# Kernel tuning notes

Measured on AMD Instinct MI355X. Metric: run time of the kernel, lower is better.

## Reference

```python
import jax, jax.numpy as jnp
import numpy as np

N, E, B = 50000, 200000, 512
F0, H1, C2, EMB = 78, 10, 128, 128
SEQ, VOCAB, NF, KW = 1000, 26, 32, 8
LOUT = EMB - KW + 1  # 121


def setup_inputs() -> dict:
    key = jax.random.key(0)
    ks = jax.random.split(key, 20)
    nrm = lambda k, s: jax.random.normal(k, s, jnp.float32) * 0.05
    return dict(
        x=jax.random.normal(ks[0], (N, F0), jnp.float32),
        edge_index=jax.random.randint(ks[1], (2, E), 0, N),
        batch=(jnp.arange(N) * B) // N,  # balanced sorted node->graph ids, all segments non-empty
        target=jax.random.randint(ks[2], (B, SEQ), 0, VOCAB),
        W1=nrm(ks[3], (F0, H1 * F0)), a_src1=nrm(ks[4], (H1, F0)), a_dst1=nrm(ks[5], (H1, F0)), b1=jnp.zeros((H1 * F0,), jnp.float32),
        W2=nrm(ks[6], (H1 * F0, C2)), a_src2=nrm(ks[7], (1, C2)), a_dst2=nrm(ks[8], (1, C2)), b2=jnp.zeros((C2,), jnp.float32),
        fc_g1_w=nrm(ks[9], (C2, C2)), fc_g1_b=jnp.zeros((C2,), jnp.float32),
        emb=nrm(ks[10], (VOCAB, EMB)),
        conv_w=nrm(ks[11], (NF, SEQ, KW)), conv_b=jnp.zeros((NF,), jnp.float32),
        fc_xt_w=nrm(ks[12], (NF * LOUT, C2)), fc_xt_b=jnp.zeros((C2,), jnp.float32),
        fc1_w=nrm(ks[13], (2 * C2, 1024)), fc1_b=jnp.zeros((1024,), jnp.float32),
        fc2_w=nrm(ks[14], (1024, 256)), fc2_b=jnp.zeros((256,), jnp.float32),
        out_w=nrm(ks[15], (256, 1)), out_b=jnp.zeros((1,), jnp.float32),
    )


def gat_conv(x, src, dst, W, a_src, a_dst, b, heads):
    # PyG GATConv (eval mode): project, per-edge attn logits, segment softmax over dst, scatter-add
    n = x.shape[0]
    c = W.shape[1] // heads
    h = (x @ W).reshape(n, heads, c)                 # [N,H,C]
    al_s = (h * a_src).sum(-1)                       # [N,H]
    al_d = (h * a_dst).sum(-1)
    al = jax.nn.leaky_relu(al_s[src] + al_d[dst], 0.2)   # [E',H]
    amax = jax.ops.segment_max(al, dst, num_segments=n)
    ex = jnp.exp(al - amax[dst])
    den = jax.ops.segment_sum(ex, dst, num_segments=n)
    alpha = ex / (den[dst] + 1e-16)
    out = jax.ops.segment_sum(h[src] * alpha[:, :, None], dst, num_segments=n)  # [N,H,C]
    return out.reshape(n, heads * c) + b


def reference(x, edge_index, batch, target, W1, a_src1, a_dst1, b1, W2, a_src2, a_dst2, b2,
              fc_g1_w, fc_g1_b, emb, conv_w, conv_b, fc_xt_w, fc_xt_b,
              fc1_w, fc1_b, fc2_w, fc2_b, out_w, out_b):
    n = x.shape[0]
    loops = jnp.arange(n)
    src = jnp.concatenate([edge_index[0], loops])    # add self loops (PyG default)
    dst = jnp.concatenate([edge_index[1], loops])
    h = jax.nn.elu(gat_conv(x, src, dst, W1, a_src1, a_dst1, b1, H1))
    h = jax.nn.relu(gat_conv(h, src, dst, W2, a_src2, a_dst2, b2, 1))
    g = jax.ops.segment_max(h, batch, num_segments=B)            # global max pool per graph
    g = jax.nn.relu(g @ fc_g1_w + fc_g1_b)                       # [B,128]
    e = emb[target]                                              # [B,1000,128]
    conv = jax.lax.conv_general_dilated(e, conv_w, (1,), 'VALID',
                                        dimension_numbers=('NCH', 'OIH', 'NCH'))
    conv = jax.nn.relu(conv + conv_b[None, :, None])             # [B,32,121]
    xt = conv.reshape(B, NF * LOUT) @ fc_xt_w + fc_xt_b          # [B,128]
    xc = jnp.concatenate([g, xt], axis=1)                        # [B,256]
    xc = jax.nn.relu(xc @ fc1_w + fc1_b)
    xc = jax.nn.relu(xc @ fc2_w + fc2_b)
    return xc @ out_w + out_b                                    # [B,1]
```

## Files before the change

### kernel.cpp

```cpp
#include <hip/hip_runtime.h>
#include <hip/hip_bf16.h>

#define N_NODES 50000
#define N_EDGES 200000
#define BGRAPHS 512
#define F0c 78
#define H1c 10
#define HC1 780
#define HSTR 832
#define C2c 128
#define SEQc 1000
#define VOCABc 26
#define NFc 32
#define KWc 8
#define LOUTc 121
#define EMBc 128
#define KX 96
#define KXT 3872
#define KSTEPS2 13
#define MROWS 13312
#define KM 1024

typedef __attribute__((ext_vector_type(8))) short short8;
typedef __attribute__((ext_vector_type(4))) float f32x4;
typedef unsigned short u16;

static constexpr size_t alignup(size_t x) { return (x + 255) & ~size_t(255); }

static constexpr size_t A_HBUF = 0;
static constexpr size_t A_OUT1 = alignup(A_HBUF + size_t(N_NODES)*HSTR*2);
static constexpr size_t A_H2   = alignup(A_OUT1 + size_t(N_NODES)*HSTR*2);
static constexpr size_t A_W2T  = alignup(A_H2   + size_t(N_NODES)*C2c*4);
static constexpr size_t A_ALS1 = alignup(A_W2T  + size_t(C2c)*HSTR*2);
static constexpr size_t A_ALD1 = alignup(A_ALS1 + size_t(N_NODES)*H1c*4);
static constexpr size_t A_ALS2 = alignup(A_ALD1 + size_t(N_NODES)*H1c*4);
static constexpr size_t A_ALD2 = alignup(A_ALS2 + size_t(N_NODES)*4);
static constexpr size_t A_DEG  = alignup(A_ALD2 + size_t(N_NODES)*4);
static constexpr size_t A_OFFS = alignup(A_DEG  + size_t(N_NODES)*4);
static constexpr size_t A_CUR  = alignup(A_OFFS + size_t(N_NODES+1)*4);
static constexpr size_t A_CSRC = alignup(A_CUR  + size_t(N_NODES)*4);
static constexpr size_t A_XC   = alignup(A_CSRC + size_t(N_EDGES+N_NODES)*4);
static constexpr size_t A_Y1   = alignup(A_XC   + size_t(BGRAPHS)*256*4);
static constexpr size_t A_BOFF = alignup(A_Y1   + size_t(BGRAPHS)*1024*4);
static constexpr size_t A_BPAD = alignup(A_BOFF + size_t(BGRAPHS)*(VOCABc+1)*4);
static constexpr size_t A_WXT  = alignup(A_BPAD + size_t(HSTR)*4);
static constexpr size_t A_FXP  = alignup(A_WXT  + size_t(C2c)*KXT*2);
static constexpr size_t A_W1HP = alignup(A_FXP  + size_t(11)*BGRAPHS*C2c*4);
static constexpr size_t A_WSD  = alignup(A_W1HP + size_t(10)*80*96*2);
static constexpr size_t A_CWT  = alignup(A_WSD  + size_t(2)*H1c*F0c*4);
static constexpr size_t A_END  = alignup(A_CWT  + size_t(2)*256*KM*2);

static constexpr size_t A_HFIN = A_HBUF;
static constexpr size_t A_AMAT = alignup(A_HFIN + size_t(N_NODES)*C2c*4);
static constexpr size_t A_CVO  = alignup(A_AMAT + size_t(MROWS)*256*4);
static constexpr size_t A_M    = alignup(A_CVO  + size_t(BGRAPHS)*KXT*2);
static_assert(A_M + size_t(MROWS)*KM*2 <= size_t(N_NODES)*HSTR*2, "alias A overflow");
static constexpr size_t A_XPAD = A_OUT1;
static_assert(size_t(N_NODES)*KX*2 <= size_t(N_NODES)*HSTR*2, "alias B overflow");

__device__ __forceinline__ float bflo(unsigned u) { return __uint_as_float(u << 16); }
__device__ __forceinline__ float bfhi(unsigned u) { return __uint_as_float(u & 0xffff0000u); }
__device__ __forceinline__ u16 f2bf(float v) {
    __hip_bfloat16 b = __float2bfloat16(v);
    return *(u16*)&b;
}

#define GLOAD16(g, l) __builtin_amdgcn_global_load_lds( \
    (const __attribute__((address_space(1))) void*)(g), \
    (__attribute__((address_space(3))) void*)(l), 16, 0, 0)

__global__ void k_prep(const float* __restrict__ x, const float* __restrict__ W1,
                       const float* __restrict__ W2, const float* __restrict__ b1,
                       const float* __restrict__ fcxt_w, const float* __restrict__ conv_w,
                       const float* __restrict__ a_src1, const float* __restrict__ a_dst1,
                       __hip_bfloat16* __restrict__ xpad, __hip_bfloat16* __restrict__ w1hp,
                       __hip_bfloat16* __restrict__ w2t, float* __restrict__ bpad,
                       __hip_bfloat16* __restrict__ wxt, float* __restrict__ wsd,
                       u16* __restrict__ cwt, int* __restrict__ deg) {
    int i = blockIdx.x*256 + threadIdx.x;
    const int R0 = N_NODES;
    const int R1 = R0 + N_NODES*KX;
    const int R2 = R1 + 10*80*96;
    const int R3 = R2 + C2c*HSTR;
    const int R4 = R3 + HSTR;
    const int R5 = R4 + C2c*KXT;
    const int R6 = R5 + 2*H1c*F0c;
    const int R7 = R6 + 256*KM;
    if (i < R0) {
        deg[i] = 1;
    } else if (i < R1) {
        int t = i - R0; int n = t / KX, c = t - n*KX;
        xpad[t] = __float2bfloat16(c < F0c ? x[(size_t)n*F0c + c] : 0.f);
    } else if (i < R2) {
        int t = i - R1; int hh = t / 7680, rem = t - hh*7680;
        int j = rem / 96, k = rem - j*96;
        w1hp[t] = __float2bfloat16((j < F0c && k < F0c) ? W1[(size_t)k*HC1 + hh*F0c + j] : 0.f);
    } else if (i < R3) {
        int t = i - R2; int c = t / HSTR, p = t - c*HSTR;
        int hh = p / 80, cc = p - hh*80;
        w2t[t] = __float2bfloat16((hh < H1c && cc < F0c) ? W2[(size_t)(hh*F0c + cc)*C2c + c] : 0.f);
    } else if (i < R4) {
        int p = i - R3; int hh = p / 80, cc = p - hh*80;
        bpad[p] = (hh < H1c && cc < F0c) ? b1[hh*F0c + cc] : 0.f;
    } else if (i < R5) {
        int t = i - R4; int c = t / KXT, j = t - c*KXT;
        wxt[t] = __float2bfloat16(fcxt_w[(size_t)j*C2c + c]);
    } else if (i < R6) {
        int t = i - R5; int sd = t / (H1c*F0c), rem = t - sd*(H1c*F0c);
        int hh = rem / F0c, c = rem - hh*F0c;
        const float* a = sd ? a_dst1 : a_src1;
        float v = 0.f;
        for (int j = 0; j < F0c; j++) v += W1[(size_t)c*HC1 + hh*F0c + j] * a[hh*F0c + j];
        wsd[t] = v;
    } else if (i < R7) {
        int t = i - R6; int col = t >> 10, ii = t & (KM-1);
        int o = col >> 3, k = col & 7;
        float v = (ii < SEQc) ? conv_w[((size_t)o*SEQc + ii)*KWc + k] : 0.f;
        u16 h = f2bf(v);
        float hv = __uint_as_float((unsigned)h << 16);
        cwt[(size_t)col*KM + ii] = h;
        cwt[(size_t)256*KM + (size_t)col*KM + ii] = f2bf(v - hv);
    }
}
#define PREP_TOTAL (N_NODES + N_NODES*KX + 10*80*96 + C2c*HSTR + HSTR + C2c*KXT + 2*H1c*F0c + 256*KM)

__global__ void k_count(const int* __restrict__ ei, int* deg) {
    int i = blockIdx.x*256 + threadIdx.x;
    if (i < N_EDGES) atomicAdd(&deg[ei[N_EDGES + i]], 1);
}
__global__ void k_scan(const int* __restrict__ deg, int* __restrict__ off,
                       int* __restrict__ cur, int n) {
    __shared__ int wsum[16];
    __shared__ int s_carry;
    int tid = threadIdx.x, lane = tid & 63, wid = tid >> 6;
    if (tid == 0) s_carry = 0;
    __syncthreads();
    for (int base = 0; base < n; base += 1024) {
        int i = base + tid;
        int v0 = (i < n) ? deg[i] : 0;
        int v = v0;
        for (int d = 1; d < 64; d <<= 1) { int t = __shfl_up(v, d, 64); if (lane >= d) v += t; }
        if (lane == 63) wsum[wid] = v;
        __syncthreads();
        if (wid == 0) {
            int w = (lane < 16) ? wsum[lane] : 0;
            for (int d = 1; d < 16; d <<= 1) { int t = __shfl_up(w, d, 64); if (lane >= d) w += t; }
            if (lane < 16) wsum[lane] = w;
        }
        __syncthreads();
        int wprev = (wid > 0) ? wsum[wid-1] : 0;
        int carry = s_carry;
        if (i < n) { int o = carry + wprev + (v - v0); off[i] = o; cur[i] = o; }
        __syncthreads();
        if (tid == 0) s_carry = carry + wsum[15];
        __syncthreads();
    }
    if (tid == 0) off[n] = s_carry;
}
__global__ void k_fill(const int* __restrict__ ei, int* cur, int* __restrict__ csrc) {
    int i = blockIdx.x*256 + threadIdx.x;
    if (i < N_EDGES) {
        int s = ei[i], d = ei[N_EDGES + i];
        int p = atomicAdd(&cur[d], 1);
        csrc[p] = s;
    } else if (i < N_EDGES + N_NODES) {
        int n = i - N_EDGES;
        int p = atomicAdd(&cur[n], 1);
        csrc[p] = n;
    }
}
__global__ void k_sortcsr(const int* __restrict__ offs, int* __restrict__ csrc) {
    int n = blockIdx.x*256 + threadIdx.x;
    if (n >= N_NODES) return;
    int s = offs[n], e = offs[n+1];
    for (int i = s + 1; i < e; i++) {
        int v = csrc[i];
        int j = i - 1;
        while (j >= s && csrc[j] > v) { csrc[j+1] = csrc[j]; j--; }
        csrc[j+1] = v;
    }
}

__global__ void k_att1x(const float* __restrict__ x, const float* __restrict__ wsd,
                        float* __restrict__ als, float* __restrict__ ald) {
    int i = blockIdx.x*256 + threadIdx.x;
    if (i >= N_NODES*H1c) return;
    int n = i / H1c, hh = i - n*H1c;
    const float* xr = x + (size_t)n*F0c;
    const float* ws = wsd + hh*F0c;
    const float* wd = wsd + H1c*F0c + hh*F0c;
    float s1 = 0.f, s2 = 0.f;
    for (int c = 0; c < F0c; c++) { float v = xr[c]; s1 += v*ws[c]; s2 += v*wd[c]; }
    als[i] = s1; ald[i] = s2;
}

__global__ void k_agg1x(const unsigned* __restrict__ xpu, const float* __restrict__ als,
                        const float* __restrict__ ald, const int* __restrict__ offs,
                        const int* __restrict__ csrc, unsigned* __restrict__ xaggu) {
    constexpr int H = H1c;
    int dn = blockIdx.x, lane = threadIdx.x;
    int s = offs[dn], e = offs[dn+1], deg = e - s;
    __shared__ float wexp[64*H];
    __shared__ int   ssrc[64];
    __shared__ float ms[H], dinv_s[H];

    if (deg <= 64) {
        if (lane < deg) ssrc[lane] = csrc[s + lane];
        __syncthreads();
        for (int idx = lane; idx < deg*H; idx += 64) {
            int j = idx / H, hh = idx - j*H;
            float al = als[(size_t)ssrc[j]*H + hh] + ald[(size_t)dn*H + hh];
            wexp[idx] = (al >= 0.f) ? al : 0.2f*al;
        }
        __syncthreads();
        if (lane < H) {
            float m = -1e30f;
            for (int j = 0; j < deg; j++) m = fmaxf(m, wexp[j*H + lane]);
            float den = 0.f;
            for (int j = 0; j < deg; j++) den += __expf(wexp[j*H + lane] - m);
            ms[lane] = m; dinv_s[lane] = 1.f/(den + 1e-16f);
        }
        __syncthreads();
        for (int idx = lane; idx < deg*H; idx += 64) {
            int hh = idx % H;
            wexp[idx] = __expf(wexp[idx] - ms[hh]) * dinv_s[hh];
        }
        __syncthreads();
        if (lane < 40) {
            float accL[H], accH[H];
            #pragma unroll
            for (int hh = 0; hh < H; hh++) { accL[hh] = 0.f; accH[hh] = 0.f; }
            int j = 0;
            for (; j + 1 < deg; j += 2) {
                unsigned ua = xpu[(size_t)ssrc[j]*48 + lane];
                unsigned ub = xpu[(size_t)ssrc[j+1]*48 + lane];
                float a0 = bflo(ua), a1 = bfhi(ua), b0 = bflo(ub), b1 = bfhi(ub);
                #pragma unroll
                for (int hh = 0; hh < H; hh++) {
                    float wA = wexp[j*H + hh], wB = wexp[(j+1)*H + hh];
                    accL[hh] += wA*a0 + wB*b0;
                    accH[hh] += wA*a1 + wB*b1;
                }
            }
            if (j < deg) {
                unsigned ua = xpu[(size_t)ssrc[j]*48 + lane];
                float a0 = bflo(ua), a1 = bfhi(ua);
                #pragma unroll
                for (int hh = 0; hh < H; hh++) {
                    float wA = wexp[j*H + hh];
                    accL[hh] += wA*a0;
                    accH[hh] += wA*a1;
                }
            }
            #pragma unroll
            for (int hh = 0; hh < H; hh++) {
                unsigned p = (unsigned)f2bf(accL[hh]) | ((unsigned)f2bf(accH[hh]) << 16);
                xaggu[((size_t)dn*H + hh)*40 + lane] = p;
            }
        }
    } else {
        if (lane < H) {
            float adv = ald[(size_t)dn*H + lane];
            float m = -1e30f;
            for (int j = s; j < e; j++) {
                float al = als[(size_t)csrc[j]*H + lane] + adv;
                al = (al >= 0.f) ? al : 0.2f*al;
                m = fmaxf(m, al);
            }
            float den = 0.f;
            for (int j = s; j < e; j++) {
                float al = als[(size_t)csrc[j]*H + lane] + adv;
                al = (al >= 0.f) ? al : 0.2f*al;
                den += __expf(al - m);
            }
            ms[lane] = m; dinv_s[lane] = 1.f/(den + 1e-16f);
        }
        __syncthreads();
        if (lane < 40) {
            float accL[H], accH[H];
            #pragma unroll
            for (int hh = 0; hh < H; hh++) { accL[hh] = 0.f; accH[hh] = 0.f; }
            for (int j = s; j < e; j++) {
                int sj = csrc[j];
                unsigned ua = xpu[(size_t)sj*48 + lane];
                float a0 = bflo(ua), a1 = bfhi(ua);
                #pragma unroll
                for (int hh = 0; hh < H; hh++) {
                    float al = als[(size_t)sj*H + hh] + ald[(size_t)dn*H + hh];
                    al = (al >= 0.f) ? al : 0.2f*al;
                    float a = __expf(al - ms[hh]) * dinv_s[hh];
                    accL[hh] += a*a0;
                    accH[hh] += a*a1;
                }
            }
            #pragma unroll
            for (int hh = 0; hh < H; hh++) {
                unsigned p = (unsigned)f2bf(accL[hh]) | ((unsigned)f2bf(accH[hh]) << 16);
                xaggu[((size_t)dn*H + hh)*40 + lane] = p;
            }
        }
    }
}

__global__ void __launch_bounds__(512, 1)
k_fuse12(const short* __restrict__ xagg, const short* __restrict__ w1hp,
         const float* __restrict__ bpad, const short* __restrict__ Bt,
         const float* __restrict__ a_src2, const float* __restrict__ a_dst2,
         float* __restrict__ Cout, float* __restrict__ als2, float* __restrict__ ald2) {
    __shared__ __attribute__((aligned(16))) short As[64*832];
    __shared__ __attribute__((aligned(16))) short Bs[2][128*64];
    __shared__ float sred[64][4], sredd[64][4];
    int tid = threadIdx.x;
    int wave = tid >> 6, lane = tid & 63;
    int m16 = lane & 15, quad = lane >> 4;
    int blockrow = blockIdx.x * 64;

    size_t boff2[2];
    #pragma unroll
    for (int j = 0; j < 2; j++) {
        int c = wave*64 + j*512 + lane;
        int row = c >> 3, cb = (c & 7) << 4;
        boff2[j] = (size_t)row*(HSTR*2) + (cb ^ ((row & 7) << 4));
        GLOAD16((const char*)Bt + boff2[j], &Bs[0][(wave*64 + j*512)*8]);
    }

    {
        int wg = (wave >> 1) * 16;
        int h0 = (wave & 1) * 5;
        int rowc = min(blockrow + wg + m16, N_NODES-1);
        for (int hh = h0; hh < h0 + 5; hh++) {
            const short8* arow = (const short8*)(xagg + ((size_t)rowc*H1c + hh)*80);
            f32x4 acc1[5];
            #pragma unroll
            for (int ct = 0; ct < 5; ct++) acc1[ct] = (f32x4){0.f,0.f,0.f,0.f};
            #pragma unroll
            for (int kt = 0; kt < 3; kt++) {
                short8 af = arow[kt*4 + quad];
                #pragma unroll
                for (int ct = 0; ct < 5; ct++) {
                    const short8* brow = (const short8*)(w1hp + (size_t)(hh*80 + ct*16 + m16)*96);
                    acc1[ct] = __builtin_amdgcn_mfma_f32_16x16x32_bf16(af, brow[kt*4 + quad],
                                                                      acc1[ct], 0, 0, 0);
                }
            }
            #pragma unroll
            for (int ct = 0; ct < 5; ct++) {
                int col = hh*80 + ct*16 + m16;
                float bv = bpad[col];
                #pragma unroll
                for (int r = 0; r < 4; r++) {
                    int rl = wg + quad*4 + r;
                    float v = acc1[ct][r] + bv;
                    v = (v > 0.f) ? v : (__expf(v) - 1.f);
                    *(u16*)((char*)As + rl*1664 + ((col*2) ^ ((rl & 7) << 4))) = f2bf(v);
                }
            }
        }
    }
    for (int e = tid; e < 64*32; e += 512) {
        int rl = e >> 5, cc = 800 + (e & 31);
        *(u16*)((char*)As + rl*1664 + ((cc*2) ^ ((rl & 7) << 4))) = 0;
    }
    __syncthreads();

    int rg = (wave >> 2) * 32;
    int ch = (wave & 3) * 32;
    f32x4 acc[2][2];
    #pragma unroll
    for (int wr = 0; wr < 2; wr++)
        #pragma unroll
        for (int ct = 0; ct < 2; ct++) acc[wr][ct] = (f32x4){0.f,0.f,0.f,0.f};

    int S = (m16 & 7) << 4;
    int cur = 0;
    for (int s = 0; s < KSTEPS2; s++) {
        if (s + 1 < KSTEPS2) {
            size_t kb = (size_t)(s + 1) * 128;
            #pragma unroll
            for (int j = 0; j < 2; j++)
                GLOAD16((const char*)Bt + boff2[j] + kb, &Bs[cur^1][(wave*64 + j*512)*8]);
        }
        const char* asB = (const char*)As + (size_t)s*128;
        const char* bsB = (const char*)&Bs[cur][0];
        #pragma unroll
        for (int kk = 0; kk < 2; kk++) {
            int kb2 = (kk*64 + quad*16) ^ S;
            short8 af[2], bfv[2];
            #pragma unroll
            for (int wr = 0; wr < 2; wr++)
                af[wr] = *(const short8*)(asB + (rg + wr*16 + m16)*1664 + kb2);
            #pragma unroll
            for (int ct = 0; ct < 2; ct++)
                bfv[ct] = *(const short8*)(bsB + (ch + ct*16 + m16)*128 + kb2);
            #pragma unroll
            for (int wr = 0; wr < 2; wr++)
                #pragma unroll
                for (int ct = 0; ct < 2; ct++)
                    acc[wr][ct] = __builtin_amdgcn_mfma_f32_16x16x32_bf16(af[wr], bfv[ct],
                                                                         acc[wr][ct], 0, 0, 0);
        }
        __syncthreads();
        cur ^= 1;
    }

    float asv[2], adv[2];
    #pragma unroll
    for (int ct = 0; ct < 2; ct++) {
        asv[ct] = a_src2[ch + ct*16 + m16];
        adv[ct] = a_dst2[ch + ct*16 + m16];
    }
    #pragma unroll
    for (int wr = 0; wr < 2; wr++) {
        #pragma unroll
        for (int ct = 0; ct < 2; ct++) {
            int col = ch + ct*16 + m16;
            #pragma unroll
            for (int r = 0; r < 4; r++) {
                int orow = blockrow + rg + wr*16 + quad*4 + r;
                if (orow < N_NODES) Cout[(size_t)orow*C2c + col] = acc[wr][ct][r];
            }
        }
        #pragma unroll
        for (int r = 0; r < 4; r++) {
            float s1 = 0.f, s2 = 0.f;
            #pragma unroll
            for (int ct = 0; ct < 2; ct++) { s1 += acc[wr][ct][r]*asv[ct]; s2 += acc[wr][ct][r]*adv[ct]; }
            #pragma unroll
            for (int d = 1; d < 16; d <<= 1) { s1 += __shfl_xor(s1, d, 64); s2 += __shfl_xor(s2, d, 64); }
            if (m16 == 0) {
                int rl = rg + wr*16 + quad*4 + r;
                sred[rl][wave & 3] = s1;
                sredd[rl][wave & 3] = s2;
            }
        }
    }
    __syncthreads();
    if (tid < 64) {
        int orow = blockrow + tid;
        if (orow < N_NODES) {
            als2[orow] = sred[tid][0] + sred[tid][1] + sred[tid][2] + sred[tid][3];
            ald2[orow] = sredd[tid][0] + sredd[tid][1] + sredd[tid][2] + sredd[tid][3];
        }
    }
}

__global__ void k_agg2(const float* __restrict__ h2, const float* __restrict__ als,
                       const float* __restrict__ ald, const int* __restrict__ offs,
                       const int* __restrict__ csrc, const float* __restrict__ b2,
                       float* __restrict__ out) {
    int dn = blockIdx.x, lane = threadIdx.x;
    int s = offs[dn], e = offs[dn+1], deg = e - s;
    __shared__ float wexp[128];
    __shared__ int ssrc[128];

    if (deg <= 128) {
        float adv = ald[dn];
        for (int j = lane; j < deg; j += 64) {
            int sj = csrc[s + j];
            ssrc[j] = sj;
            float al = als[sj] + adv;
            wexp[j] = (al >= 0.f) ? al : 0.2f*al;
        }
        __syncthreads();
        float m = -1e30f;
        for (int j = lane; j < deg; j += 64) m = fmaxf(m, wexp[j]);
        #pragma unroll
        for (int d = 32; d > 0; d >>= 1) m = fmaxf(m, __shfl_xor(m, d, 64));
        __syncthreads();
        float den = 0.f;
        for (int j = lane; j < deg; j += 64) {
            float ex = __expf(wexp[j] - m);
            wexp[j] = ex;
            den += ex;
        }
        #pragma unroll
        for (int d = 32; d > 0; d >>= 1) den += __shfl_xor(den, d, 64);
        float dinv = 1.f/(den + 1e-16f);
        __syncthreads();
        float2 acc = {0.f, 0.f};
        for (int j = 0; j < deg; j++) {
            float alpha = wexp[j] * dinv;
            float2 v = ((const float2*)(h2 + (size_t)ssrc[j]*C2c))[lane];
            acc.x += alpha*v.x; acc.y += alpha*v.y;
        }
        float2 o;
        o.x = fmaxf(acc.x + b2[2*lane], 0.f);
        o.y = fmaxf(acc.y + b2[2*lane+1], 0.f);
        ((float2*)(out + (size_t)dn*C2c))[lane] = o;
    } else {
        __shared__ float sm[2];
        if (lane == 0) {
            float adv = ald[dn];
            float m = -1e30f;
            for (int j = s; j < e; j++) {
                float al = als[csrc[j]] + adv;
                al = (al >= 0.f) ? al : 0.2f*al;
                m = fmaxf(m, al);
            }
            float den = 0.f;
            for (int j = s; j < e; j++) {
                float al = als[csrc[j]] + adv;
                al = (al >= 0.f) ? al : 0.2f*al;
                den += __expf(al - m);
            }
            sm[0] = m; sm[1] = 1.f/(den + 1e-16f);
        }
        __syncthreads();
        float m = sm[0], dinv = sm[1], adv = ald[dn];
        float2 acc = {0.f, 0.f};
        for (int j = s; j < e; j++) {
            int sj = csrc[j];
            float al = als[sj] + adv;
            al = (al >= 0.f) ? al : 0.2f*al;
            float alpha = __expf(al - m) * dinv;
            float2 v = ((const float2*)(h2 + (size_t)sj*C2c))[lane];
            acc.x += alpha*v.x; acc.y += alpha*v.y;
        }
        float2 o;
        o.x = fmaxf(acc.x + b2[2*lane], 0.f);
        o.y = fmaxf(acc.y + b2[2*lane+1], 0.f);
        ((float2*)(out + (size_t)dn*C2c))[lane] = o;
    }
}

__global__ void k_poolfcg(const float* __restrict__ hf, const int* __restrict__ batch,
                          const float* __restrict__ W, const float* __restrict__ bias,
                          float* __restrict__ xc) {
    int b = blockIdx.x, tid = threadIdx.x;
    __shared__ int se[2];
    __shared__ float gs[C2c];
    if (tid < 2) {
        int key = b + tid;
        int lo = 0, hi = N_NODES;
        while (lo < hi) { int mid = (lo+hi) >> 1; if (batch[mid] < key) lo = mid+1; else hi = mid; }
        se[tid] = lo;
    }
    __syncthreads();
    int s = se[0], e = se[1];
    float m = -1e30f;
    for (int n = s; n < e; n++) m = fmaxf(m, hf[(size_t)n*C2c + tid]);
    gs[tid] = m;
    __syncthreads();
    float acc = bias[tid];
    for (int k = 0; k < C2c; k++) acc += gs[k] * W[k*C2c + tid];
    xc[b*256 + tid] = fmaxf(acc, 0.f);
}

__global__ void k_buildM(const int* __restrict__ target, u16* __restrict__ Mm) {
    int b = blockIdx.x, tid = threadIdx.x;
    short8 z = (short8){0,0,0,0,0,0,0,0};
    short8* base = (short8*)(Mm + (size_t)b*VOCABc*KM);
    for (int i = tid; i < VOCABc*KM/8; i += 256) base[i] = z;
    __syncthreads();
    for (int i = tid; i < SEQc; i += 256) {
        int t = target[(size_t)b*SEQc + i];
        Mm[((size_t)b*VOCABc + t)*KM + i] = (u16)0x3F80;
    }
}

__global__ void __launch_bounds__(256, 1)
k_amat_mfma(const short* __restrict__ Mm, const short* __restrict__ cwt,
            float* __restrict__ A2) {
    __shared__ __attribute__((aligned(16))) short As[2][128*64];
    __shared__ __attribute__((aligned(16))) short Bh[2][128*64];
    __shared__ __attribute__((aligned(16))) short Bl[2][128*64];
    int tid = threadIdx.x;
    int wave = tid >> 6, lane = tid & 63;
    int m16 = lane & 15, quad = lane >> 4;
    int blockrow = blockIdx.x * 128;
    int colbase  = blockIdx.y * 128;

    size_t aoff[4], bo[4];
    #pragma unroll
    for (int i = 0; i < 4; i++) {
        int c = wave*256 + i*64 + lane;
        int row = c >> 3;
        int cb  = (c & 7) << 4;
        int srcb = cb ^ ((row & 7) << 4);
        aoff[i] = (size_t)(blockrow + row) * (KM*2) + srcb;
        bo[i]   = (size_t)(colbase  + row) * (KM*2) + srcb;
    }
    const char* hbase = (const char*)cwt;
    const char* lbase = (const char*)(cwt + (size_t)256*KM);

    f32x4 acc[2][8];
    #pragma unroll
    for (int wr = 0; wr < 2; wr++)
        #pragma unroll
        for (int ct = 0; ct < 8; ct++) acc[wr][ct] = (f32x4){0.f,0.f,0.f,0.f};

    #pragma unroll
    for (int i = 0; i < 4; i++) {
        GLOAD16((const char*)Mm + aoff[i], &As[0][(wave*256 + i*64)*8]);
        GLOAD16(hbase + bo[i],             &Bh[0][(wave*256 + i*64)*8]);
        GLOAD16(lbase + bo[i],             &Bl[0][(wave*256 + i*64)*8]);
    }
    __syncthreads();

    int cur = 0;
    int S = (m16 & 7) << 4;
    for (int s = 0; s < KM/64; s++) {
        if (s + 1 < KM/64) {
            size_t kb = (size_t)(s + 1) * 128;
            #pragma unroll
            for (int i = 0; i < 4; i++) {
                GLOAD16((const char*)Mm + aoff[i] + kb, &As[cur^1][(wave*256 + i*64)*8]);
                GLOAD16(hbase + bo[i] + kb,             &Bh[cur^1][(wave*256 + i*64)*8]);
                GLOAD16(lbase + bo[i] + kb,             &Bl[cur^1][(wave*256 + i*64)*8]);
            }
        }
        const char* asBase = (const char*)&As[cur][0];
        const char* bhBase = (const char*)&Bh[cur][0];
        const char* blBase = (const char*)&Bl[cur][0];
        #pragma unroll
        for (int kk = 0; kk < 2; kk++) {
            int kb2 = (kk*64 + quad*16) ^ S;
            short8 af[2];
            #pragma unroll
            for (int wr = 0; wr < 2; wr++) {
                int row = wave*32 + wr*16 + m16;
                af[wr] = *(const short8*)(asBase + row*128 + kb2);
            }
            #pragma unroll
            for (int ct = 0; ct < 8; ct++) {
                int col = ct*16 + m16;
                short8 bhv = *(const short8*)(bhBase + col*128 + kb2);
                short8 blv = *(const short8*)(blBase + col*128 + kb2);
                acc[0][ct] = __builtin_amdgcn_mfma_f32_16x16x32_bf16(af[0], bhv, acc[0][ct], 0, 0, 0);
                acc[1][ct] = __builtin_amdgcn_mfma_f32_16x16x32_bf16(af[1], bhv, acc[1][ct], 0, 0, 0);
                acc[0][ct] = __builtin_amdgcn_mfma_f32_16x16x32_bf16(af[0], blv, acc[0][ct], 0, 0, 0);
                acc[1][ct] = __builtin_amdgcn_mfma_f32_16x16x32_bf16(af[1], blv, acc[1][ct], 0, 0, 0);
            }
        }
        __syncthreads();
        cur ^= 1;
    }

    #pragma unroll
    for (int wr = 0; wr < 2; wr++) {
        int rowbase = blockrow + wave*32 + wr*16 + quad*4;
        #pragma unroll
        for (int ct = 0; ct < 8; ct++) {
            int col = colbase + ct*16 + m16;
            #pragma unroll
            for (int r = 0; r < 4; r++) {
                A2[(size_t)(rowbase + r)*256 + col] = acc[wr][ct][r];
            }
        }
    }
}

__global__ void __launch_bounds__(128, 4)
k_conv(const float* __restrict__ A2, const float* __restrict__ emb,
       const float* __restrict__ convb, u16* __restrict__ convout) {
    int b = blockIdx.x, og = blockIdx.y;
    int tid = threadIdx.x;
    __shared__ float embs[VOCABc*EMBc];
    __shared__ float arow[4*VOCABc*KWc];
    for (int i = tid; i < VOCABc*EMBc; i += 128) embs[i] = emb[i];
    for (int i = tid; i < 4*VOCABc*KWc; i += 128) {
        int o2 = i / (VOCABc*KWc);
        int rem = i - o2*(VOCABc*KWc);
        int t = rem >> 3, k = rem & 7;
        arow[i] = A2[((size_t)b*VOCABc + t)*256 + (og*4 + o2)*8 + k];
    }
    __syncthreads();
    if (tid < LOUTc) {
        float a0 = convb[og*4+0], a1 = convb[og*4+1], a2 = convb[og*4+2], a3 = convb[og*4+3];
        for (int t = 0; t < VOCABc; t++) {
            #pragma unroll
            for (int k = 0; k < KWc; k++) {
                float ev = embs[t*EMBc + tid + k];
                a0 += arow[0*(VOCABc*KWc) + t*KWc + k] * ev;
                a1 += arow[1*(VOCABc*KWc) + t*KWc + k] * ev;
                a2 += arow[2*(VOCABc*KWc) + t*KWc + k] * ev;
                a3 += arow[3*(VOCABc*KWc) + t*KWc + k] * ev;
            }
        }
        size_t base = (size_t)b*KXT + (og*4)*LOUTc + tid;
        convout[base            ] = f2bf(fmaxf(a0, 0.f));
        convout[base +   LOUTc  ] = f2bf(fmaxf(a1, 0.f));
        convout[base + 2*LOUTc  ] = f2bf(fmaxf(a2, 0.f));
        convout[base + 3*LOUTc  ] = f2bf(fmaxf(a3, 0.f));
    }
}
__global__ void k_fcxt_mfma(const short* __restrict__ cvo, const short* __restrict__ wxt,
                            float* __restrict__ fxp) {
    int wave = threadIdx.x >> 6, lane = threadIdx.x & 63;
    int m16 = lane & 15, quad = lane >> 4;
    int r0 = blockIdx.x*64 + wave*16;
    int kt0 = blockIdx.y*11;
    const short8* arow = (const short8*)(cvo + (size_t)(r0 + m16)*KXT);
    f32x4 acc[8];
    #pragma unroll
    for (int ct = 0; ct < 8; ct++) acc[ct] = (f32x4){0.f,0.f,0.f,0.f};
    for (int kt = kt0; kt < kt0 + 11; kt++) {
        short8 af = arow[kt*4 + quad];
        #pragma unroll
        for (int ct = 0; ct < 8; ct++) {
            const short8* brow = (const short8*)(wxt + (size_t)(ct*16 + m16)*KXT);
            short8 bf = brow[kt*4 + quad];
            acc[ct] = __builtin_amdgcn_mfma_f32_16x16x32_bf16(af, bf, acc[ct], 0, 0, 0);
        }
    }
    #pragma unroll
    for (int ct = 0; ct < 8; ct++) {
        int col = ct*16 + m16;
        #pragma unroll
        for (int r = 0; r < 4; r++) {
            int row = r0 + quad*4 + r;
            fxp[((size_t)blockIdx.y*BGRAPHS + row)*C2c + col] = acc[ct][r];
        }
    }
}

__global__ void k_fc1(const float* __restrict__ xc, const float* __restrict__ fxp,
                      const float* __restrict__ fcxt_b, const float* __restrict__ W,
                      const float* __restrict__ bias, float* __restrict__ y1) {
    int b = blockIdx.x, tid = threadIdx.x;
    __shared__ float xs[256];
    if (tid < 128) {
        xs[tid] = xc[b*256 + tid];
    } else {
        int col = tid - 128;
        float s = fcxt_b[col];
        #pragma unroll
        for (int q = 0; q < 11; q++) s += fxp[((size_t)q*BGRAPHS + b)*C2c + col];
        xs[tid] = s;
    }
    __syncthreads();
    float a0 = bias[tid], a1 = bias[tid+256], a2 = bias[tid+512], a3 = bias[tid+768];
    for (int k = 0; k < 256; k++) {
        float xk = xs[k];
        const float* wr = W + (size_t)k*1024;
        a0 += xk*wr[tid]; a1 += xk*wr[tid+256]; a2 += xk*wr[tid+512]; a3 += xk*wr[tid+768];
    }
    y1[(size_t)b*1024 + tid      ] = fmaxf(a0, 0.f);
    y1[(size_t)b*1024 + tid + 256] = fmaxf(a1, 0.f);
    y1[(size_t)b*1024 + tid + 512] = fmaxf(a2, 0.f);
    y1[(size_t)b*1024 + tid + 768] = fmaxf(a3, 0.f);
}
__global__ void k_fc2out(const float* __restrict__ y1, const float* __restrict__ W,
                         const float* __restrict__ bias, const float* __restrict__ ow,
                         const float* __restrict__ ob, float* __restrict__ out) {
    int b = blockIdx.x, tid = threadIdx.x;
    int lane = tid & 63, wid = tid >> 6;
    __shared__ float ys[1024];
    __shared__ float wsum[4];
    for (int i = tid; i < 1024; i += 256) ys[i] = y1[(size_t)b*1024 + i];
    __syncthreads();
    float acc = bias[tid];
    for (int k = 0; k < 1024; k++) acc += ys[k] * W[(size_t)k*256 + tid];
    float v = fmaxf(acc, 0.f) * ow[tid];
    #pragma unroll
    for (int d = 32; d > 0; d >>= 1) v += __shfl_xor(v, d, 64);
    if (lane == 0) wsum[wid] = v;
    __syncthreads();
    if (tid == 0) out[b] = wsum[0] + wsum[1] + wsum[2] + wsum[3] + ob[0];
}

extern "C" void kernel_launch(void* const* d_in, const int* in_sizes, int n_in,
                              void* d_out, int out_size, void* d_ws, size_t ws_size,
                              hipStream_t stream) {
    (void)in_sizes; (void)n_in; (void)out_size;
    if (ws_size < A_END) return;

    const float* x       = (const float*)d_in[0];
    const int*   ei      = (const int*)  d_in[1];
    const int*   batch   = (const int*)  d_in[2];
    const int*   target  = (const int*)  d_in[3];
    const float* W1      = (const float*)d_in[4];
    const float* a_src1  = (const float*)d_in[5];
    const float* a_dst1  = (const float*)d_in[6];
    const float* b1      = (const float*)d_in[7];
    const float* W2      = (const float*)d_in[8];
    const float* a_src2  = (const float*)d_in[9];
    const float* a_dst2  = (const float*)d_in[10];
    const float* b2      = (const float*)d_in[11];
    const float* fcg_w   = (const float*)d_in[12];
    const float* fcg_b   = (const float*)d_in[13];
    const float* emb     = (const float*)d_in[14];
    const float* conv_w  = (const float*)d_in[15];
    const float* conv_b  = (const float*)d_in[16];
    const float* fcxt_w  = (const float*)d_in[17];
    const float* fcxt_b  = (const float*)d_in[18];
    const float* fc1_w   = (const float*)d_in[19];
    const float* fc1_b   = (const float*)d_in[20];
    const float* fc2_w   = (const float*)d_in[21];
    const float* fc2_b   = (const float*)d_in[22];
    const float* out_w   = (const float*)d_in[23];
    const float* out_b   = (const float*)d_in[24];

    char* wsb = (char*)d_ws;
    u16*   xagg  = (u16*)  (wsb + A_HBUF);
    float* h2    = (float*)(wsb + A_H2);
    __hip_bfloat16* w2t = (__hip_bfloat16*)(wsb + A_W2T);
    float* als1  = (float*)(wsb + A_ALS1);
    float* ald1  = (float*)(wsb + A_ALD1);
    float* als2  = (float*)(wsb + A_ALS2);
    float* ald2  = (float*)(wsb + A_ALD2);
    int*   deg   = (int*)  (wsb + A_DEG);
    int*   offs  = (int*)  (wsb + A_OFFS);
    int*   cur   = (int*)  (wsb + A_CUR);
    int*   csrc  = (int*)  (wsb + A_CSRC);
    float* xc    = (float*)(wsb + A_XC);
    float* y1    = (float*)(wsb + A_Y1);
    float* bpad  = (float*)(wsb + A_BPAD);
    __hip_bfloat16* wxt  = (__hip_bfloat16*)(wsb + A_WXT);
    float* fxp   = (float*)(wsb + A_FXP);
    __hip_bfloat16* w1hp = (__hip_bfloat16*)(wsb + A_W1HP);
    float* wsd   = (float*)(wsb + A_WSD);
    u16*   cwt   = (u16*)  (wsb + A_CWT);
    float* hfin  = (float*)(wsb + A_HFIN);
    float* Amat2 = (float*)(wsb + A_AMAT);
    u16*   cvo   = (u16*)  (wsb + A_CVO);
    u16*   Mm    = (u16*)  (wsb + A_M);
    __hip_bfloat16* xpad = (__hip_bfloat16*)(wsb + A_XPAD);

    k_prep<<<(PREP_TOTAL+255)/256, 256, 0, stream>>>(x, W1, W2, b1, fcxt_w, conv_w,
                                                     a_src1, a_dst1,
                                                     xpad, w1hp, w2t, bpad, wxt, wsd, cwt, deg);
    k_count  <<<(N_EDGES+255)/256, 256, 0, stream>>>(ei, deg);
    k_scan   <<<1, 1024, 0, stream>>>(deg, offs, cur, N_NODES);
    k_fill   <<<(N_EDGES+N_NODES+255)/256, 256, 0, stream>>>(ei, cur, csrc);
    k_sortcsr<<<(N_NODES+255)/256, 256, 0, stream>>>(offs, csrc);

    k_att1x<<<(N_NODES*H1c+255)/256, 256, 0, stream>>>(x, wsd, als1, ald1);
    k_agg1x<<<N_NODES, 64, 0, stream>>>((const unsigned*)xpad, als1, ald1, offs, csrc,
                                        (unsigned*)xagg);

    k_fuse12<<<(N_NODES+63)/64, 512, 0, stream>>>((const short*)xagg, (const short*)w1hp,
                                                  bpad, (const short*)w2t,
                                                  a_src2, a_dst2, h2, als2, ald2);

    k_buildM<<<BGRAPHS, 256, 0, stream>>>(target, Mm);

    k_agg2<<<N_NODES, 64, 0, stream>>>(h2, als2, ald2, offs, csrc, b2, hfin);

    k_poolfcg<<<BGRAPHS, 128, 0, stream>>>(hfin, batch, fcg_w, fcg_b, xc);

    k_amat_mfma<<<dim3(MROWS/128, 2), 256, 0, stream>>>((const short*)Mm, (const short*)cwt,
                                                        Amat2);
    k_conv  <<<dim3(BGRAPHS, 8), 128, 0, stream>>>(Amat2, emb, conv_b, cvo);
    k_fcxt_mfma<<<dim3(BGRAPHS/64, 11), 256, 0, stream>>>((const short*)cvo, (const short*)wxt, fxp);

    k_fc1<<<BGRAPHS, 256, 0, stream>>>(xc, fxp, fcxt_b, fc1_w, fc1_b, y1);
    k_fc2out<<<BGRAPHS, 256, 0, stream>>>(y1, fc2_w, fc2_b, out_w, out_b, (float*)d_out);
}
```

Measured before the change: 574.2 us.

## Shrink fuse12 tile to 32 rows, read fragment-packed W2 directly from global

The fused layer-1/layer-2 GEMM kernel now handles 32 rows per block instead of 64. It drops the double-buffered LDS staging of W2 and reads B fragments directly from a new MFMA-fragment-ordered W2 layout prepared in k_prep. The K loop is trimmed to the 800 real columns, so the zero-padding pass over columns 800-831 goes away, and launch bounds now allow 4 blocks per CU. LDS use falls sharply, which should raise occupancy and hide latency. The trade-off is that every wave reloads the full W2 fragments from global or L2 with no LDS reuse.

```diff
diff --git a/kernel.cpp b/kernel.cpp
--- a/kernel.cpp
+++ b/kernel.cpp
@@ -17,9 +17,9 @@
 #define EMBc 128
 #define KX 96
 #define KXT 3872
-#define KSTEPS2 13
 #define MROWS 13312
 #define KM 1024
+#define W2TF_N (25*8*64*8)
 
 typedef __attribute__((ext_vector_type(8))) short short8;
 typedef __attribute__((ext_vector_type(4))) float f32x4;
@@ -49,6 +49,7 @@
 static constexpr size_t A_WSD  = alignup(A_W1HP + size_t(10)*80*96*2);
 static constexpr size_t A_CWT  = alignup(A_WSD  + size_t(2)*H1c*F0c*4);
 static constexpr size_t A_END  = alignup(A_CWT  + size_t(2)*256*KM*2);
+static_assert(W2TF_N*2 <= size_t(C2c)*HSTR*2, "w2tf fits old slot");
 
 static constexpr size_t A_HFIN = A_HBUF;
 static constexpr size_t A_AMAT = alignup(A_HFIN + size_t(N_NODES)*C2c*4);
@@ -74,14 +75,14 @@
                        const float* __restrict__ fcxt_w, const float* __restrict__ conv_w,
                        const float* __restrict__ a_src1, const float* __restrict__ a_dst1,
                        __hip_bfloat16* __restrict__ xpad, __hip_bfloat16* __restrict__ w1hp,
-                       __hip_bfloat16* __restrict__ w2t, float* __restrict__ bpad,
+                       u16* __restrict__ w2tf, float* __restrict__ bpad,
                        __hip_bfloat16* __restrict__ wxt, float* __restrict__ wsd,
                        u16* __restrict__ cwt, int* __restrict__ deg) {
     int i = blockIdx.x*256 + threadIdx.x;
     const int R0 = N_NODES;
     const int R1 = R0 + N_NODES*KX;
     const int R2 = R1 + 10*80*96;
-    const int R3 = R2 + C2c*HSTR;
+    const int R3 = R2 + W2TF_N;
     const int R4 = R3 + HSTR;
     const int R5 = R4 + C2c*KXT;
     const int R6 = R5 + 2*H1c*F0c;
@@ -96,9 +97,12 @@
         int j = rem / 96, k = rem - j*96;
         w1hp[t] = __float2bfloat16((j < F0c && k < F0c) ? W1[(size_t)k*HC1 + hh*F0c + j] : 0.f);
     } else if (i < R3) {
-        int t = i - R2; int c = t / HSTR, p = t - c*HSTR;
-        int hh = p / 80, cc = p - hh*80;
-        w2t[t] = __float2bfloat16((hh < H1c && cc < F0c) ? W2[(size_t)(hh*F0c + cc)*C2c + c] : 0.f);
+        int t = i - R2; int frag = t >> 3, tt = t & 7;
+        int m16 = frag & 15, quad = (frag >> 4) & 3, cbg = (frag >> 6) & 7, kstep = frag >> 9;
+        int col = cbg*16 + m16;
+        int k = kstep*32 + quad*8 + tt;
+        int hh = k / 80, cc = k - hh*80;
+        w2tf[t] = f2bf((cc < F0c) ? W2[(size_t)(hh*F0c + cc)*C2c + col] : 0.f);
     } else if (i < R4) {
         int p = i - R3; int hh = p / 80, cc = p - hh*80;
         bpad[p] = (hh < H1c && cc < F0c) ? b1[hh*F0c + cc] : 0.f;
@@ -122,7 +126,7 @@
         cwt[(size_t)256*KM + (size_t)col*KM + ii] = f2bf(v - hv);
     }
 }
-#define PREP_TOTAL (N_NODES + N_NODES*KX + 10*80*96 + C2c*HSTR + HSTR + C2c*KXT + 2*H1c*F0c + 256*KM)
+#define PREP_TOTAL (N_NODES + N_NODES*KX + 10*80*96 + W2TF_N + HSTR + C2c*KXT + 2*H1c*F0c + 256*KM)
 
 __global__ void k_count(const int* __restrict__ ei, int* deg) {
     int i = blockIdx.x*256 + threadIdx.x;
@@ -302,33 +306,23 @@
     }
 }
 
-__global__ void __launch_bounds__(512, 1)
+__global__ void __launch_bounds__(512, 4)
 k_fuse12(const short* __restrict__ xagg, const short* __restrict__ w1hp,
-         const float* __restrict__ bpad, const short* __restrict__ Bt,
+         const float* __restrict__ bpad, const short* __restrict__ w2tf,
          const float* __restrict__ a_src2, const float* __restrict__ a_dst2,
          float* __restrict__ Cout, float* __restrict__ als2, float* __restrict__ ald2) {
-    __shared__ __attribute__((aligned(16))) short As[64*832];
-    __shared__ __attribute__((aligned(16))) short Bs[2][128*64];
-    __shared__ float sred[64][4], sredd[64][4];
+    __shared__ __attribute__((aligned(16))) short As[32*832];
+    __shared__ float sred[32][4], sredd[32][4];
     int tid = threadIdx.x;
     int wave = tid >> 6, lane = tid & 63;
     int m16 = lane & 15, quad = lane >> 4;
-    int blockrow = blockIdx.x * 64;
-
-    size_t boff2[2];
-    #pragma unroll
-    for (int j = 0; j < 2; j++) {
-        int c = wave*64 + j*512 + lane;
-        int row = c >> 3, cb = (c & 7) << 4;
-        boff2[j] = (size_t)row*(HSTR*2) + (cb ^ ((row & 7) << 4));
-        GLOAD16((const char*)Bt + boff2[j], &Bs[0][(wave*64 + j*512)*8]);
-    }
+    int blockrow = blockIdx.x * 32;
+    int rg = wave >> 2;
 
     {
-        int wg = (wave >> 1) * 16;
-        int h0 = (wave & 1) * 5;
-        int rowc = min(blockrow + wg + m16, N_NODES-1);
-        for (int hh = h0; hh < h0 + 5; hh++) {
+        int hg = wave & 3;
+        int rowc = min(blockrow + rg*16 + m16, N_NODES-1);
+        for (int hh = hg; hh < H1c; hh += 4) {
             const short8* arow = (const short8*)(xagg + ((size_t)rowc*H1c + hh)*80);
             f32x4 acc1[5];
             #pragma unroll
@@ -349,7 +343,7 @@
                 float bv = bpad[col];
                 #pragma unroll
                 for (int r = 0; r < 4; r++) {
-                    int rl = wg + quad*4 + r;
+                    int rl = rg*16 + quad*4 + r;
                     float v = acc1[ct][r] + bv;
                     v = (v > 0.f) ? v : (__expf(v) - 1.f);
                     *(u16*)((char*)As + rl*1664 + ((col*2) ^ ((rl & 7) << 4))) = f2bf(v);
@@ -357,85 +351,54 @@
             }
         }
     }
-    for (int e = tid; e < 64*32; e += 512) {
-        int rl = e >> 5, cc = 800 + (e & 31);
-        *(u16*)((char*)As + rl*1664 + ((cc*2) ^ ((rl & 7) << 4))) = 0;
-    }
-    __syncthreads();
-
-    int rg = (wave >> 2) * 32;
-    int ch = (wave & 3) * 32;
-    f32x4 acc[2][2];
-    #pragma unroll
-    for (int wr = 0; wr < 2; wr++)
-        #pragma unroll
-        for (int ct = 0; ct < 2; ct++) acc[wr][ct] = (f32x4){0.f,0.f,0.f,0.f};
-
+    __syncthreads();
+
+    int cg = wave & 3;
+    f32x4 acc[2];
+    acc[0] = (f32x4){0.f,0.f,0.f,0.f};
+    acc[1] = (f32x4){0.f,0.f,0.f,0.f};
     int S = (m16 & 7) << 4;
-    int cur = 0;
-    for (int s = 0; s < KSTEPS2; s++) {
-        if (s + 1 < KSTEPS2) {
-            size_t kb = (size_t)(s + 1) * 128;
-            #pragma unroll
-            for (int j = 0; j < 2; j++)
-                GLOAD16((const char*)Bt + boff2[j] + kb, &Bs[cur^1][(wave*64 + j*512)*8]);
-        }
-        const char* asB = (const char*)As + (size_t)s*128;
-        const char* bsB = (const char*)&Bs[cur][0];
-        #pragma unroll
-        for (int kk = 0; kk < 2; kk++) {
-            int kb2 = (kk*64 + quad*16) ^ S;
-            short8 af[2], bfv[2];
-            #pragma unroll
-            for (int wr = 0; wr < 2; wr++)
-                af[wr] = *(const short8*)(asB + (rg + wr*16 + m16)*1664 + kb2);
-            #pragma unroll
-            for (int ct = 0; ct < 2; ct++)
-                bfv[ct] = *(const short8*)(bsB + (ch + ct*16 + m16)*128 + kb2);
-            #pragma unroll
-            for (int wr = 0; wr < 2; wr++)
-                #pragma unroll
-                for (int ct = 0; ct < 2; ct++)
-                    acc[wr][ct] = __builtin_amdgcn_mfma_f32_16x16x32_bf16(af[wr], bfv[ct],
-                                                                         acc[wr][ct], 0, 0, 0);
-        }
-        __syncthreads();
-        cur ^= 1;
+    const char* asRow = (const char*)As + (size_t)(rg*16 + m16)*1664;
+    const short8* bp = (const short8*)w2tf;
+    #pragma unroll 5
+    for (int kstep = 0; kstep < 25; kstep++) {
+        short8 af = *(const short8*)(asRow + ((kstep*64 + quad*16) ^ S));
+        short8 b0 = bp[(size_t)(kstep*8 + cg*2    )*64 + lane];
+        short8 b1 = bp[(size_t)(kstep*8 + cg*2 + 1)*64 + lane];
+        acc[0] = __builtin_amdgcn_mfma_f32_16x16x32_bf16(af, b0, acc[0], 0, 0, 0);
+        acc[1] = __builtin_amdgcn_mfma_f32_16x16x32_bf16(af, b1, acc[1], 0, 0, 0);
     }
 
     float asv[2], adv[2];
     #pragma unroll
     for (int ct = 0; ct < 2; ct++) {
-        asv[ct] = a_src2[ch + ct*16 + m16];
-        adv[ct] = a_dst2[ch + ct*16 + m16];
-    }
-    #pragma unroll
-    for (int wr = 0; wr < 2; wr++) {
-        #pragma unroll
-        for (int ct = 0; ct < 2; ct++) {
-            int col = ch + ct*16 + m16;
-            #pragma unroll
-            for (int r = 0; r < 4; r++) {
-                int orow = blockrow + rg + wr*16 + quad*4 + r;
-                if (orow < N_NODES) Cout[(size_t)orow*C2c + col] = acc[wr][ct][r];
-            }
-        }
+        asv[ct] = a_src2[cg*32 + ct*16 + m16];
+        adv[ct] = a_dst2[cg*32 + ct*16 + m16];
+    }
+    #pragma unroll
+    for (int ct = 0; ct < 2; ct++) {
+        int col = cg*32 + ct*16 + m16;
         #pragma unroll
         for (int r = 0; r < 4; r++) {
-            float s1 = 0.f, s2 = 0.f;
-            #pragma unroll
-            for (int ct = 0; ct < 2; ct++) { s1 += acc[wr][ct][r]*asv[ct]; s2 += acc[wr][ct][r]*adv[ct]; }
-            #pragma unroll
-            for (int d = 1; d < 16; d <<= 1) { s1 += __shfl_xor(s1, d, 64); s2 += __shfl_xor(s2, d, 64); }
-            if (m16 == 0) {
-                int rl = rg + wr*16 + quad*4 + r;
-                sred[rl][wave & 3] = s1;
-                sredd[rl][wave & 3] = s2;
-            }
-        }
-    }
-    __syncthreads();
-    if (tid < 64) {
+            int orow = blockrow + rg*16 + quad*4 + r;
+            if (orow < N_NODES) Cout[(size_t)orow*C2c + col] = acc[ct][r];
+        }
+    }
+    #pragma unroll
+    for (int r = 0; r < 4; r++) {
+        float s1 = 0.f, s2 = 0.f;
+        #pragma unroll
+        for (int ct = 0; ct < 2; ct++) { s1 += acc[ct][r]*asv[ct]; s2 += acc[ct][r]*adv[ct]; }
+        #pragma unroll
+        for (int d = 1; d < 16; d <<= 1) { s1 += __shfl_xor(s1, d, 64); s2 += __shfl_xor(s2, d, 64); }
+        if (m16 == 0) {
+            int rl = rg*16 + quad*4 + r;
+            sred[rl][cg] = s1;
+            sredd[rl][cg] = s2;
+        }
+    }
+    __syncthreads();
+    if (tid < 32) {
         int orow = blockrow + tid;
         if (orow < N_NODES) {
             als2[orow] = sred[tid][0] + sred[tid][1] + sred[tid][2] + sred[tid][3];
@@ -794,7 +757,7 @@
     char* wsb = (char*)d_ws;
     u16*   xagg  = (u16*)  (wsb + A_HBUF);
     float* h2    = (float*)(wsb + A_H2);
-    __hip_bfloat16* w2t = (__hip_bfloat16*)(wsb + A_W2T);
+    u16*   w2tf  = (u16*)  (wsb + A_W2T);
     float* als1  = (float*)(wsb + A_ALS1);
     float* ald1  = (float*)(wsb + A_ALD1);
     float* als2  = (float*)(wsb + A_ALS2);
@@ -819,7 +782,7 @@
 
     k_prep<<<(PREP_TOTAL+255)/256, 256, 0, stream>>>(x, W1, W2, b1, fcxt_w, conv_w,
                                                      a_src1, a_dst1,
-                                                     xpad, w1hp, w2t, bpad, wxt, wsd, cwt, deg);
+                                                     xpad, w1hp, w2tf, bpad, wxt, wsd, cwt, deg);
     k_count  <<<(N_EDGES+255)/256, 256, 0, stream>>>(ei, deg);
     k_scan   <<<1, 1024, 0, stream>>>(deg, offs, cur, N_NODES);
     k_fill   <<<(N_EDGES+N_NODES+255)/256, 256, 0, stream>>>(ei, cur, csrc);
@@ -829,8 +792,8 @@
     k_agg1x<<<N_NODES, 64, 0, stream>>>((const unsigned*)xpad, als1, ald1, offs, csrc,
                                         (unsigned*)xagg);
 
-    k_fuse12<<<(N_NODES+63)/64, 512, 0, stream>>>((const short*)xagg, (const short*)w1hp,
-                                                  bpad, (const short*)w2t,
+    k_fuse12<<<(N_NODES+31)/32, 512, 0, stream>>>((const short*)xagg, (const short*)w1hp,
+                                                  bpad, (const short*)w2tf,
                                                   a_src2, a_dst2, h2, als2, ald2);
 
     k_buildM<<<BGRAPHS, 256, 0, stream>>>(target, Mm);
```

Measured after the change: 531.1 us. -7.5%, faster.
